# Optimization experiments

Hardware: AMD Instinct MI355X
Metric: run time of the kernel (lower is better)

The kernel has to match this reference:

```python
import jax, jax.numpy as jnp
import numpy as np


def setup_inputs() -> dict:
    key = jax.random.key(0)
    ks = jax.random.split(key, 7)
    B, N, D, A = 32, 128, 512, 512
    sD = 1.0 / np.sqrt(D)
    sA = 1.0 / np.sqrt(A)
    return {
        "x": jax.random.normal(ks[0], (B, N, D), dtype=jnp.float32),
        "W1": jax.random.normal(ks[1], (A, D), dtype=jnp.float32) * sD,
        "b1": jax.random.normal(ks[2], (A,), dtype=jnp.float32) * sD,
        "W2": jax.random.normal(ks[3], (A, D), dtype=jnp.float32) * sD,
        "b2": jax.random.normal(ks[4], (A,), dtype=jnp.float32) * sD,
        "Wout": jax.random.normal(ks[5], (A,), dtype=jnp.float32) * sA,
        "bout": jax.random.normal(ks[6], (1,), dtype=jnp.float32) * sA,
    }


def reference(x, W1, b1, W2, b2, Wout, bout):
    # x: (B, N, D)
    x1 = jnp.einsum('bnd,ad->bna', x, W1) + b1  # mlp1 -> (B, N, A)
    x2 = jnp.einsum('bnd,ad->bna', x, W2) + b2  # mlp2 -> (B, N, A)
    # outer broadcast add: x1.unsqueeze(1) + x2.unsqueeze(2) -> (B, N, N, A)
    s = x1[:, None, :, :] + x2[:, :, None, :]
    # include_root=False: drop ROOT row along dim 1 -> (B, N-1, N, A)
    s = s[:, 1:, :, :]
    s = jnp.tanh(s)
    # out linear A -> 1, then squeeze -> (B, N-1, N)
    return jnp.einsum('bija,a->bij', s, Wout) + bout[0]
```

## Files before the change

kernel.cpp:

```cpp
#include <hip/hip_runtime.h>
#include <hip/hip_bf16.h>

#define B_ 32
#define N_ 128
#define D_ 512
#define A_ 512
#define R_ (B_*N_)
#define OC 1024
#define CEXP 2.8853900817779268f

typedef __attribute__((ext_vector_type(8))) short  frag_ab;
typedef __attribute__((ext_vector_type(4))) float  frag_cd;

__device__ inline unsigned pack2bf(float a, float b) {
    unsigned ua = __builtin_bit_cast(unsigned, a) + 0x8000u;
    unsigned ub = __builtin_bit_cast(unsigned, b) + 0x8000u;
    return __builtin_amdgcn_perm(ub, ua, 0x07060302);
}
__device__ inline float bf2f_lo(unsigned u){ return __builtin_bit_cast(float, u << 16); }
__device__ inline float bf2f_hi(unsigned u){ return __builtin_bit_cast(float, u & 0xffff0000u); }

__global__ __launch_bounds__(256) void k0_cvt(
    const float* __restrict__ X, const float* __restrict__ W1,
    const float* __restrict__ W2,
    unsigned short* __restrict__ Xb, unsigned short* __restrict__ W1b,
    unsigned short* __restrict__ W2b)
{
    const int NX = R_*D_/8, NW = A_*D_/8;
    int i = blockIdx.x*256 + threadIdx.x;
    const float* src; unsigned short* dst; int off;
    if (i < NX)            { src = X;  dst = Xb;  off = i; }
    else if (i < NX+NW)    { src = W1; dst = W1b; off = i-NX; }
    else if (i < NX+2*NW)  { src = W2; dst = W2b; off = i-NX-NW; }
    else return;
    float4 a = ((const float4*)src)[off*2];
    float4 c = ((const float4*)src)[off*2+1];
    uint4 o;
    o.x = pack2bf(a.x,a.y); o.y = pack2bf(a.z,a.w);
    o.z = pack2bf(c.x,c.y); o.w = pack2bf(c.z,c.w);
    ((uint4*)dst)[off] = o;
}

#define BK1 64
#define LDK 68

__global__ __launch_bounds__(256) void k1_mfma(
    const unsigned short* __restrict__ Xb,
    const unsigned short* __restrict__ W1b, const float* __restrict__ b1,
    const unsigned short* __restrict__ W2b, const float* __restrict__ b2,
    unsigned short* __restrict__ Yb)
{
    __shared__ unsigned short As[2][128*LDK];
    __shared__ unsigned short Bs[2][128*LDK];

    const int t = threadIdx.x, lane = t&63, wid = t>>6;
    const int wr = wid>>1, wc = wid&1;
    const int row0 = blockIdx.x*128, col0 = blockIdx.y*128;
    const unsigned short* Wb = (col0 < A_) ? W1b : W2b;
    const float* bb = (col0 < A_) ? b1 : b2;
    const int wrow0 = col0 & (A_-1);

    const int srow = t>>3;
    const int scol = (t&7)*8;

    frag_cd acc[4][4];
#pragma unroll
    for (int i=0;i<4;++i)
#pragma unroll
        for (int j=0;j<4;++j) acc[i][j] = frag_cd{0.f,0.f,0.f,0.f};

    const int fr = lane&15, g8 = (lane>>4)*8;

    uint4 ra[4], rb[4];
#pragma unroll
    for (int q=0;q<4;++q){
        int r = q*32 + srow;
        ra[q] = *(const uint4*)&Xb[(size_t)(row0 +r)*D_ + scol];
        rb[q] = *(const uint4*)&Wb[(size_t)(wrow0+r)*D_ + scol];
    }
#pragma unroll
    for (int q=0;q<4;++q){
        int r = q*32 + srow;
        *(uint4*)&As[0][r*LDK + scol] = ra[q];
        *(uint4*)&Bs[0][r*LDK + scol] = rb[q];
    }
    __syncthreads();

#pragma unroll
    for (int s=0; s<8; ++s) {
        const int cur = s&1;
        if (s<7) {
            const int k0 = (s+1)*BK1;
#pragma unroll
            for (int q=0;q<4;++q){
                int r = q*32 + srow;
                ra[q] = *(const uint4*)&Xb[(size_t)(row0 +r)*D_ + k0 + scol];
                rb[q] = *(const uint4*)&Wb[(size_t)(wrow0+r)*D_ + k0 + scol];
            }
        }
        frag_ab af[4][2], bf[4][2];
#pragma unroll
        for (int fi=0;fi<4;++fi)
#pragma unroll
            for (int ks=0;ks<2;++ks) {
                af[fi][ks] = *(const frag_ab*)&As[cur][(wr*64+fi*16+fr)*LDK + ks*32 + g8];
                bf[fi][ks] = *(const frag_ab*)&Bs[cur][(wc*64+fi*16+fr)*LDK + ks*32 + g8];
            }
#pragma unroll
        for (int ks=0;ks<2;++ks)
#pragma unroll
            for (int fi=0;fi<4;++fi)
#pragma unroll
                for (int fj=0;fj<4;++fj)
                    acc[fi][fj] = __builtin_amdgcn_mfma_f32_16x16x32_bf16(
                        af[fi][ks], bf[fj][ks], acc[fi][fj], 0, 0, 0);
        if (s<7) {
#pragma unroll
            for (int q=0;q<4;++q){
                int r = q*32 + srow;
                *(uint4*)&As[cur^1][r*LDK + scol] = ra[q];
                *(uint4*)&Bs[cur^1][r*LDK + scol] = rb[q];
            }
        }
        __syncthreads();
    }

#pragma unroll
    for (int fi=0;fi<4;++fi){
        const int rr = row0 + wr*64 + fi*16 + (lane>>4)*4;
#pragma unroll
        for (int fj=0;fj<4;++fj){
            const int cc = col0 + wc*64 + fj*16 + (lane&15);
            const float bias = bb[cc & (A_-1)];
#pragma unroll
            for (int r=0;r<4;++r){
                float e = __builtin_amdgcn_exp2f(CEXP*(acc[fi][fj][r] + bias));
                Yb[(size_t)(rr+r)*OC + cc] =
                    (unsigned short)((__builtin_bit_cast(unsigned, e) + 0x8000u) >> 16);
            }
        }
    }
}

#define ACH 128
#define LDA2 (ACH+4)

__global__ __launch_bounds__(256) void k2_tanh(
    const unsigned short* __restrict__ Yb,
    const float* __restrict__ Wout, const float* __restrict__ bout,
    float* __restrict__ out)
{
    __shared__ float e1s[2][32][LDA2];
    __shared__ float e2s[2][32][LDA2];
    __shared__ float wo[A_];
    __shared__ float wsum_s[4];

    const int t  = threadIdx.x;
    const int jt = blockIdx.x, it = blockIdx.y, b = blockIdx.z;

    float wsacc = 0.f;
    for (int k=t; k<A_; k+=256){ float w = Wout[k]; wo[k] = w; wsacc += w; }
#pragma unroll
    for (int off=32; off>=1; off>>=1) wsacc += __shfl_down(wsacc, off, 64);
    if ((t&63)==0) wsum_s[t>>6] = wsacc;

    const unsigned short* yb = Yb + (size_t)b*N_*OC;
    const int sr = t>>4;
    const int sc = (t&15)*8;

    uint4 r1[2], r2[2];
#pragma unroll
    for (int q=0;q<2;++q){
        int row = q*16 + sr;
        r1[q] = *(const uint4*)&yb[(size_t)(jt*32+row)*OC + sc];
        int i2 = it*32 + row + 1; if (i2 > 127) i2 = 127;
        r2[q] = *(const uint4*)&yb[(size_t)i2*OC + A_ + sc];
    }
#pragma unroll
    for (int q=0;q<2;++q){
        int row = q*16 + sr;
        uint4 v = r1[q];
        float4 lo = {bf2f_lo(v.x), bf2f_hi(v.x), bf2f_lo(v.y), bf2f_hi(v.y)};
        float4 hi = {bf2f_lo(v.z), bf2f_hi(v.z), bf2f_lo(v.w), bf2f_hi(v.w)};
        *(float4*)&e1s[0][row][sc]   = lo;
        *(float4*)&e1s[0][row][sc+4] = hi;
        v = r2[q];
        float4 lo2 = {bf2f_lo(v.x), bf2f_hi(v.x), bf2f_lo(v.y), bf2f_hi(v.y)};
        float4 hi2 = {bf2f_lo(v.z), bf2f_hi(v.z), bf2f_lo(v.w), bf2f_hi(v.w)};
        *(float4*)&e2s[0][row][sc]   = lo2;
        *(float4*)&e2s[0][row][sc+4] = hi2;
    }
    __syncthreads();

    const int jl = t&15, il = t>>4;
    float a00=0.f, a01=0.f, a10=0.f, a11=0.f;

#pragma unroll
    for (int ch=0; ch<4; ++ch) {
        const int cur = ch&1;
        if (ch<3) {
            const int a0n = (ch+1)*ACH;
#pragma unroll
            for (int q=0;q<2;++q){
                int row = q*16 + sr;
                r1[q] = *(const uint4*)&yb[(size_t)(jt*32+row)*OC + a0n + sc];
                int i2 = it*32 + row + 1; if (i2 > 127) i2 = 127;
                r2[q] = *(const uint4*)&yb[(size_t)i2*OC + A_ + a0n + sc];
            }
        }
        const int a0 = ch*ACH;
#pragma unroll 4
        for (int c=0; c<ACH; c+=4) {
            float4 u0 = *(const float4*)&e1s[cur][jl     ][c];
            float4 u1 = *(const float4*)&e1s[cur][jl + 16][c];
            float4 v0 = *(const float4*)&e2s[cur][il     ][c];
            float4 v1 = *(const float4*)&e2s[cur][il + 16][c];
            float4 w  = *(const float4*)&wo[a0 + c];
            a00 += w.x * __builtin_amdgcn_rcpf(fmaf(u0.x, v0.x, 1.f));
            a01 += w.x * __builtin_amdgcn_rcpf(fmaf(u1.x, v0.x, 1.f));
            a10 += w.x * __builtin_amdgcn_rcpf(fmaf(u0.x, v1.x, 1.f));
            a11 += w.x * __builtin_amdgcn_rcpf(fmaf(u1.x, v1.x, 1.f));
            a00 += w.y * __builtin_amdgcn_rcpf(fmaf(u0.y, v0.y, 1.f));
            a01 += w.y * __builtin_amdgcn_rcpf(fmaf(u1.y, v0.y, 1.f));
            a10 += w.y * __builtin_amdgcn_rcpf(fmaf(u0.y, v1.y, 1.f));
            a11 += w.y * __builtin_amdgcn_rcpf(fmaf(u1.y, v1.y, 1.f));
            a00 += w.z * __builtin_amdgcn_rcpf(fmaf(u0.z, v0.z, 1.f));
            a01 += w.z * __builtin_amdgcn_rcpf(fmaf(u1.z, v0.z, 1.f));
            a10 += w.z * __builtin_amdgcn_rcpf(fmaf(u0.z, v1.z, 1.f));
            a11 += w.z * __builtin_amdgcn_rcpf(fmaf(u1.z, v1.z, 1.f));
            a00 += w.w * __builtin_amdgcn_rcpf(fmaf(u0.w, v0.w, 1.f));
            a01 += w.w * __builtin_amdgcn_rcpf(fmaf(u1.w, v0.w, 1.f));
            a10 += w.w * __builtin_amdgcn_rcpf(fmaf(u0.w, v1.w, 1.f));
            a11 += w.w * __builtin_amdgcn_rcpf(fmaf(u1.w, v1.w, 1.f));
        }
        if (ch<3) {
#pragma unroll
            for (int q=0;q<2;++q){
                int row = q*16 + sr;
                uint4 v = r1[q];
                float4 lo = {bf2f_lo(v.x), bf2f_hi(v.x), bf2f_lo(v.y), bf2f_hi(v.y)};
                float4 hi = {bf2f_lo(v.z), bf2f_hi(v.z), bf2f_lo(v.w), bf2f_hi(v.w)};
                *(float4*)&e1s[cur^1][row][sc]   = lo;
                *(float4*)&e1s[cur^1][row][sc+4] = hi;
                v = r2[q];
                float4 lo2 = {bf2f_lo(v.x), bf2f_hi(v.x), bf2f_lo(v.y), bf2f_hi(v.y)};
                float4 hi2 = {bf2f_lo(v.z), bf2f_hi(v.z), bf2f_lo(v.w), bf2f_hi(v.w)};
                *(float4*)&e2s[cur^1][row][sc]   = lo2;
                *(float4*)&e2s[cur^1][row][sc+4] = hi2;
            }
            __syncthreads();
        }
    }

    const float wsum = wsum_s[0] + wsum_s[1] + wsum_s[2] + wsum_s[3];
    const float bo   = bout[0];
    const int i0 = it*32 + il;
    const int j0 = jt*32 + jl;

    if (i0 < 127)      out[((size_t)(b*127) + i0     ) * 128 + j0     ] = wsum - 2.f*a00 + bo;
    if (i0 < 127)      out[((size_t)(b*127) + i0     ) * 128 + j0 + 16] = wsum - 2.f*a01 + bo;
    if (i0 + 16 < 127) out[((size_t)(b*127) + i0 + 16) * 128 + j0     ] = wsum - 2.f*a10 + bo;
    if (i0 + 16 < 127) out[((size_t)(b*127) + i0 + 16) * 128 + j0 + 16] = wsum - 2.f*a11 + bo;
}

extern "C" void kernel_launch(void* const* d_in, const int* in_sizes, int n_in,
                              void* d_out, int out_size, void* d_ws, size_t ws_size,
                              hipStream_t stream) {
    const float* x    = (const float*)d_in[0];
    const float* W1   = (const float*)d_in[1];
    const float* b1   = (const float*)d_in[2];
    const float* W2   = (const float*)d_in[3];
    const float* b2   = (const float*)d_in[4];
    const float* Wout = (const float*)d_in[5];
    const float* bout = (const float*)d_in[6];
    float* out = (float*)d_out;

    char* ws = (char*)d_ws;
    unsigned short* Yb  = (unsigned short*)ws;
    unsigned short* Xb  = (unsigned short*)(ws + (8u<<20));
    unsigned short* W1b = (unsigned short*)(ws + (12u<<20));
    unsigned short* W2b = (unsigned short*)(ws + (12u<<20) + (1u<<19));

    k0_cvt<<<1280, 256, 0, stream>>>(x, W1, W2, Xb, W1b, W2b);

    dim3 g1(R_/128, OC/128);
    k1_mfma<<<g1, 256, 0, stream>>>(Xb, W1b, b1, W2b, b2, Yb);

    dim3 g2(4, 4, B_);
    k2_tanh<<<g2, 256, 0, stream>>>(Yb, Wout, bout, out);
}
```

Before: 131.1 us.

## Halve GEMM and tanh-reduction tiles to launch more blocks

The MFMA projection kernel drops from 128x128 to 64x64 output tiles, so it launches four times as many blocks. The pairwise tanh kernel shrinks its i-tile from 32 to 16 rows, doubling its grid, and replaces the double-buffered shared memory with a single buffer and an extra barrier. The aim is to fill the MI355X's many compute units and cut register and LDS pressure. In exchange, each tile of Y is reloaded from global memory more often, there is less work per thread, and the tanh kernel no longer overlaps its shared-memory writes with compute.

```diff
diff --git a/kernel.cpp b/kernel.cpp
--- a/kernel.cpp
+++ b/kernel.cpp
@@ -50,12 +50,12 @@
     const unsigned short* __restrict__ W2b, const float* __restrict__ b2,
     unsigned short* __restrict__ Yb)
 {
-    __shared__ unsigned short As[2][128*LDK];
-    __shared__ unsigned short Bs[2][128*LDK];
+    __shared__ unsigned short As[2][64*LDK];
+    __shared__ unsigned short Bs[2][64*LDK];
 
     const int t = threadIdx.x, lane = t&63, wid = t>>6;
     const int wr = wid>>1, wc = wid&1;
-    const int row0 = blockIdx.x*128, col0 = blockIdx.y*128;
+    const int row0 = blockIdx.x*64, col0 = blockIdx.y*64;
     const unsigned short* Wb = (col0 < A_) ? W1b : W2b;
     const float* bb = (col0 < A_) ? b1 : b2;
     const int wrow0 = col0 & (A_-1);
@@ -63,23 +63,23 @@
     const int srow = t>>3;
     const int scol = (t&7)*8;
 
-    frag_cd acc[4][4];
-#pragma unroll
-    for (int i=0;i<4;++i)
-#pragma unroll
-        for (int j=0;j<4;++j) acc[i][j] = frag_cd{0.f,0.f,0.f,0.f};
+    frag_cd acc[2][2];
+#pragma unroll
+    for (int i=0;i<2;++i)
+#pragma unroll
+        for (int j=0;j<2;++j) acc[i][j] = frag_cd{0.f,0.f,0.f,0.f};
 
     const int fr = lane&15, g8 = (lane>>4)*8;
 
-    uint4 ra[4], rb[4];
-#pragma unroll
-    for (int q=0;q<4;++q){
+    uint4 ra[2], rb[2];
+#pragma unroll
+    for (int q=0;q<2;++q){
         int r = q*32 + srow;
         ra[q] = *(const uint4*)&Xb[(size_t)(row0 +r)*D_ + scol];
         rb[q] = *(const uint4*)&Wb[(size_t)(wrow0+r)*D_ + scol];
     }
 #pragma unroll
-    for (int q=0;q<4;++q){
+    for (int q=0;q<2;++q){
         int r = q*32 + srow;
         *(uint4*)&As[0][r*LDK + scol] = ra[q];
         *(uint4*)&Bs[0][r*LDK + scol] = rb[q];
@@ -92,31 +92,31 @@
         if (s<7) {
             const int k0 = (s+1)*BK1;
 #pragma unroll
-            for (int q=0;q<4;++q){
+            for (int q=0;q<2;++q){
                 int r = q*32 + srow;
                 ra[q] = *(const uint4*)&Xb[(size_t)(row0 +r)*D_ + k0 + scol];
                 rb[q] = *(const uint4*)&Wb[(size_t)(wrow0+r)*D_ + k0 + scol];
             }
         }
-        frag_ab af[4][2], bf[4][2];
-#pragma unroll
-        for (int fi=0;fi<4;++fi)
+        frag_ab af[2][2], bf[2][2];
+#pragma unroll
+        for (int fi=0;fi<2;++fi)
 #pragma unroll
             for (int ks=0;ks<2;++ks) {
-                af[fi][ks] = *(const frag_ab*)&As[cur][(wr*64+fi*16+fr)*LDK + ks*32 + g8];
-                bf[fi][ks] = *(const frag_ab*)&Bs[cur][(wc*64+fi*16+fr)*LDK + ks*32 + g8];
+                af[fi][ks] = *(const frag_ab*)&As[cur][(wr*32+fi*16+fr)*LDK + ks*32 + g8];
+                bf[fi][ks] = *(const frag_ab*)&Bs[cur][(wc*32+fi*16+fr)*LDK + ks*32 + g8];
             }
 #pragma unroll
         for (int ks=0;ks<2;++ks)
 #pragma unroll
-            for (int fi=0;fi<4;++fi)
-#pragma unroll
-                for (int fj=0;fj<4;++fj)
+            for (int fi=0;fi<2;++fi)
+#pragma unroll
+                for (int fj=0;fj<2;++fj)
                     acc[fi][fj] = __builtin_amdgcn_mfma_f32_16x16x32_bf16(
                         af[fi][ks], bf[fj][ks], acc[fi][fj], 0, 0, 0);
         if (s<7) {
 #pragma unroll
-            for (int q=0;q<4;++q){
+            for (int q=0;q<2;++q){
                 int r = q*32 + srow;
                 *(uint4*)&As[cur^1][r*LDK + scol] = ra[q];
                 *(uint4*)&Bs[cur^1][r*LDK + scol] = rb[q];
@@ -126,11 +126,11 @@
     }
 
 #pragma unroll
-    for (int fi=0;fi<4;++fi){
-        const int rr = row0 + wr*64 + fi*16 + (lane>>4)*4;
-#pragma unroll
-        for (int fj=0;fj<4;++fj){
-            const int cc = col0 + wc*64 + fj*16 + (lane&15);
+    for (int fi=0;fi<2;++fi){
+        const int rr = row0 + wr*32 + fi*16 + (lane>>4)*4;
+#pragma unroll
+        for (int fj=0;fj<2;++fj){
+            const int cc = col0 + wc*32 + fj*16 + (lane&15);
             const float bias = bb[cc & (A_-1)];
 #pragma unroll
             for (int r=0;r<4;++r){
@@ -150,13 +150,15 @@
     const float* __restrict__ Wout, const float* __restrict__ bout,
     float* __restrict__ out)
 {
-    __shared__ float e1s[2][32][LDA2];
-    __shared__ float e2s[2][32][LDA2];
+    __shared__ float e1s[32][LDA2];
+    __shared__ float e2s[16][LDA2];
     __shared__ float wo[A_];
     __shared__ float wsum_s[4];
 
     const int t  = threadIdx.x;
-    const int jt = blockIdx.x, it = blockIdx.y, b = blockIdx.z;
+    const int jt = blockIdx.x;
+    const int it = blockIdx.y;
+    const int b  = blockIdx.z;
 
     float wsacc = 0.f;
     for (int k=t; k<A_; k+=256){ float w = Wout[k]; wo[k] = w; wsacc += w; }
@@ -168,99 +170,74 @@
     const int sr = t>>4;
     const int sc = (t&15)*8;
 
-    uint4 r1[2], r2[2];
-#pragma unroll
-    for (int q=0;q<2;++q){
-        int row = q*16 + sr;
-        r1[q] = *(const uint4*)&yb[(size_t)(jt*32+row)*OC + sc];
-        int i2 = it*32 + row + 1; if (i2 > 127) i2 = 127;
-        r2[q] = *(const uint4*)&yb[(size_t)i2*OC + A_ + sc];
-    }
-#pragma unroll
-    for (int q=0;q<2;++q){
-        int row = q*16 + sr;
-        uint4 v = r1[q];
-        float4 lo = {bf2f_lo(v.x), bf2f_hi(v.x), bf2f_lo(v.y), bf2f_hi(v.y)};
-        float4 hi = {bf2f_lo(v.z), bf2f_hi(v.z), bf2f_lo(v.w), bf2f_hi(v.w)};
-        *(float4*)&e1s[0][row][sc]   = lo;
-        *(float4*)&e1s[0][row][sc+4] = hi;
-        v = r2[q];
-        float4 lo2 = {bf2f_lo(v.x), bf2f_hi(v.x), bf2f_lo(v.y), bf2f_hi(v.y)};
-        float4 hi2 = {bf2f_lo(v.z), bf2f_hi(v.z), bf2f_lo(v.w), bf2f_hi(v.w)};
-        *(float4*)&e2s[0][row][sc]   = lo2;
-        *(float4*)&e2s[0][row][sc+4] = hi2;
+    uint4 p1a = *(const uint4*)&yb[(size_t)(jt*32 + sr     )*OC + sc];
+    uint4 p1b = *(const uint4*)&yb[(size_t)(jt*32 + sr + 16)*OC + sc];
+    int i2c = it*16 + sr + 1; if (i2c > 127) i2c = 127;
+    uint4 p2  = *(const uint4*)&yb[(size_t)i2c*OC + A_ + sc];
+    {
+        uint4 v = p1a;
+        *(float4*)&e1s[sr][sc]   = float4{bf2f_lo(v.x),bf2f_hi(v.x),bf2f_lo(v.y),bf2f_hi(v.y)};
+        *(float4*)&e1s[sr][sc+4] = float4{bf2f_lo(v.z),bf2f_hi(v.z),bf2f_lo(v.w),bf2f_hi(v.w)};
+        v = p1b;
+        *(float4*)&e1s[sr+16][sc]   = float4{bf2f_lo(v.x),bf2f_hi(v.x),bf2f_lo(v.y),bf2f_hi(v.y)};
+        *(float4*)&e1s[sr+16][sc+4] = float4{bf2f_lo(v.z),bf2f_hi(v.z),bf2f_lo(v.w),bf2f_hi(v.w)};
+        v = p2;
+        *(float4*)&e2s[sr][sc]   = float4{bf2f_lo(v.x),bf2f_hi(v.x),bf2f_lo(v.y),bf2f_hi(v.y)};
+        *(float4*)&e2s[sr][sc+4] = float4{bf2f_lo(v.z),bf2f_hi(v.z),bf2f_lo(v.w),bf2f_hi(v.w)};
     }
     __syncthreads();
 
     const int jl = t&15, il = t>>4;
-    float a00=0.f, a01=0.f, a10=0.f, a11=0.f;
+    float a00 = 0.f, a01 = 0.f;
 
 #pragma unroll
     for (int ch=0; ch<4; ++ch) {
-        const int cur = ch&1;
         if (ch<3) {
             const int a0n = (ch+1)*ACH;
-#pragma unroll
-            for (int q=0;q<2;++q){
-                int row = q*16 + sr;
-                r1[q] = *(const uint4*)&yb[(size_t)(jt*32+row)*OC + a0n + sc];
-                int i2 = it*32 + row + 1; if (i2 > 127) i2 = 127;
-                r2[q] = *(const uint4*)&yb[(size_t)i2*OC + A_ + a0n + sc];
-            }
+            p1a = *(const uint4*)&yb[(size_t)(jt*32 + sr     )*OC + a0n + sc];
+            p1b = *(const uint4*)&yb[(size_t)(jt*32 + sr + 16)*OC + a0n + sc];
+            p2  = *(const uint4*)&yb[(size_t)i2c*OC + A_ + a0n + sc];
         }
         const int a0 = ch*ACH;
 #pragma unroll 4
         for (int c=0; c<ACH; c+=4) {
-            float4 u0 = *(const float4*)&e1s[cur][jl     ][c];
-            float4 u1 = *(const float4*)&e1s[cur][jl + 16][c];
-            float4 v0 = *(const float4*)&e2s[cur][il     ][c];
-            float4 v1 = *(const float4*)&e2s[cur][il + 16][c];
+            float4 u0 = *(const float4*)&e1s[jl     ][c];
+            float4 u1 = *(const float4*)&e1s[jl + 16][c];
+            float4 v0 = *(const float4*)&e2s[il     ][c];
             float4 w  = *(const float4*)&wo[a0 + c];
             a00 += w.x * __builtin_amdgcn_rcpf(fmaf(u0.x, v0.x, 1.f));
             a01 += w.x * __builtin_amdgcn_rcpf(fmaf(u1.x, v0.x, 1.f));
-            a10 += w.x * __builtin_amdgcn_rcpf(fmaf(u0.x, v1.x, 1.f));
-            a11 += w.x * __builtin_amdgcn_rcpf(fmaf(u1.x, v1.x, 1.f));
             a00 += w.y * __builtin_amdgcn_rcpf(fmaf(u0.y, v0.y, 1.f));
             a01 += w.y * __builtin_amdgcn_rcpf(fmaf(u1.y, v0.y, 1.f));
-            a10 += w.y * __builtin_amdgcn_rcpf(fmaf(u0.y, v1.y, 1.f));
-            a11 += w.y * __builtin_amdgcn_rcpf(fmaf(u1.y, v1.y, 1.f));
             a00 += w.z * __builtin_amdgcn_rcpf(fmaf(u0.z, v0.z, 1.f));
             a01 += w.z * __builtin_amdgcn_rcpf(fmaf(u1.z, v0.z, 1.f));
-            a10 += w.z * __builtin_amdgcn_rcpf(fmaf(u0.z, v1.z, 1.f));
-            a11 += w.z * __builtin_amdgcn_rcpf(fmaf(u1.z, v1.z, 1.f));
             a00 += w.w * __builtin_amdgcn_rcpf(fmaf(u0.w, v0.w, 1.f));
             a01 += w.w * __builtin_amdgcn_rcpf(fmaf(u1.w, v0.w, 1.f));
-            a10 += w.w * __builtin_amdgcn_rcpf(fmaf(u0.w, v1.w, 1.f));
-            a11 += w.w * __builtin_amdgcn_rcpf(fmaf(u1.w, v1.w, 1.f));
         }
         if (ch<3) {
-#pragma unroll
-            for (int q=0;q<2;++q){
-                int row = q*16 + sr;
-                uint4 v = r1[q];
-                float4 lo = {bf2f_lo(v.x), bf2f_hi(v.x), bf2f_lo(v.y), bf2f_hi(v.y)};
-                float4 hi = {bf2f_lo(v.z), bf2f_hi(v.z), bf2f_lo(v.w), bf2f_hi(v.w)};
-                *(float4*)&e1s[cur^1][row][sc]   = lo;
-                *(float4*)&e1s[cur^1][row][sc+4] = hi;
-                v = r2[q];
-                float4 lo2 = {bf2f_lo(v.x), bf2f_hi(v.x), bf2f_lo(v.y), bf2f_hi(v.y)};
-                float4 hi2 = {bf2f_lo(v.z), bf2f_hi(v.z), bf2f_lo(v.w), bf2f_hi(v.w)};
-                *(float4*)&e2s[cur^1][row][sc]   = lo2;
-                *(float4*)&e2s[cur^1][row][sc+4] = hi2;
-            }
+            __syncthreads();
+            uint4 v = p1a;
+            *(float4*)&e1s[sr][sc]   = float4{bf2f_lo(v.x),bf2f_hi(v.x),bf2f_lo(v.y),bf2f_hi(v.y)};
+            *(float4*)&e1s[sr][sc+4] = float4{bf2f_lo(v.z),bf2f_hi(v.z),bf2f_lo(v.w),bf2f_hi(v.w)};
+            v = p1b;
+            *(float4*)&e1s[sr+16][sc]   = float4{bf2f_lo(v.x),bf2f_hi(v.x),bf2f_lo(v.y),bf2f_hi(v.y)};
+            *(float4*)&e1s[sr+16][sc+4] = float4{bf2f_lo(v.z),bf2f_hi(v.z),bf2f_lo(v.w),bf2f_hi(v.w)};
+            v = p2;
+            *(float4*)&e2s[sr][sc]   = float4{bf2f_lo(v.x),bf2f_hi(v.x),bf2f_lo(v.y),bf2f_hi(v.y)};
+            *(float4*)&e2s[sr][sc+4] = float4{bf2f_lo(v.z),bf2f_hi(v.z),bf2f_lo(v.w),bf2f_hi(v.w)};
             __syncthreads();
         }
     }
 
     const float wsum = wsum_s[0] + wsum_s[1] + wsum_s[2] + wsum_s[3];
     const float bo   = bout[0];
-    const int i0 = it*32 + il;
+    const int i0 = it*16 + il;
     const int j0 = jt*32 + jl;
 
-    if (i0 < 127)      out[((size_t)(b*127) + i0     ) * 128 + j0     ] = wsum - 2.f*a00 + bo;
-    if (i0 < 127)      out[((size_t)(b*127) + i0     ) * 128 + j0 + 16] = wsum - 2.f*a01 + bo;
-    if (i0 + 16 < 127) out[((size_t)(b*127) + i0 + 16) * 128 + j0     ] = wsum - 2.f*a10 + bo;
-    if (i0 + 16 < 127) out[((size_t)(b*127) + i0 + 16) * 128 + j0 + 16] = wsum - 2.f*a11 + bo;
+    if (i0 < 127) {
+        out[((size_t)(b*127) + i0) * 128 + j0     ] = wsum - 2.f*a00 + bo;
+        out[((size_t)(b*127) + i0) * 128 + j0 + 16] = wsum - 2.f*a01 + bo;
+    }
 }
 
 extern "C" void kernel_launch(void* const* d_in, const int* in_sizes, int n_in,
@@ -283,9 +260,9 @@
 
     k0_cvt<<<1280, 256, 0, stream>>>(x, W1, W2, Xb, W1b, W2b);
 
-    dim3 g1(R_/128, OC/128);
+    dim3 g1(R_/64, OC/64);
     k1_mfma<<<g1, 256, 0, stream>>>(Xb, W1b, b1, W2b, b2, Yb);
 
-    dim3 g2(4, 4, B_);
+    dim3 g2(4, 8, B_);
     k2_tanh<<<g2, 256, 0, stream>>>(Yb, Wout, bout, out);
 }
```

After: 115.6 us. 11.8% less time.
